# Kernel optimization log

Measured on AMD Instinct MI355X. Metric: run time of the kernel, lower is better.

## Reference

```python
import jax, jax.numpy as jnp
import numpy as np

B, T, IN, R = 256, 512, 64, 2048
SPECTRAL_RADIUS = 0.9


def setup_inputs() -> dict:
    key = jax.random.key(0)
    k1, k2 = jax.random.split(key)
    X = jax.random.normal(k1, (B, T, IN), dtype=jnp.float32)
    rng = np.random.default_rng(0)
    Win = rng.standard_normal((R, IN)).astype(np.float32)
    W = rng.standard_normal((R, R))
    eigs = np.abs(np.linalg.eigvals(W))
    W = (W / np.max(eigs) * SPECTRAL_RADIUS).astype(np.float32)
    return {"X": X, "Win": jnp.asarray(Win), "W": jnp.asarray(W)}


def reference(X, Win, W):
    def step(s, x_t):
        # s: [B, R], x_t: [B, IN]
        s_new = jnp.tanh(x_t @ Win.T + s @ W.T)
        return s_new, None

    s0 = jnp.zeros((X.shape[0], W.shape[0]), dtype=X.dtype)
    xs = jnp.swapaxes(X, 0, 1)  # [T, B, IN]
    s_final, _ = jax.lax.scan(step, s0, xs)
    return s_final  # [B, R]
```

## Files before the change

### kernel.cpp

```cpp
#include <hip/hip_runtime.h>
#include <hip/hip_fp16.h>
#include <cmath>

constexpr int kB  = 256;
constexpr int kT  = 512;
constexpr int kIN = 64;
constexpr int kR  = 2048;

constexpr int kBands  = 8;
constexpr int kNB     = 32;
constexpr int kBlocks = kBands * kNB;
constexpr int BM = 32;
constexpr int BN = 64;
constexpr int PFS = 68;

typedef _Float16 f16x8 __attribute__((ext_vector_type(8)));
typedef float    f32x4 __attribute__((ext_vector_type(4)));
typedef unsigned long long u64;

#define MFMA16(a, b, c) __builtin_amdgcn_mfma_f32_16x16x32_f16((a), (b), (c), 0, 0, 0)

__device__ __forceinline__ f16x8 cvt8(float4 a, float4 b) {
    f16x8 v;
    v[0] = (_Float16)a.x; v[1] = (_Float16)a.y; v[2] = (_Float16)a.z; v[3] = (_Float16)a.w;
    v[4] = (_Float16)b.x; v[5] = (_Float16)b.y; v[6] = (_Float16)b.z; v[7] = (_Float16)b.w;
    return v;
}

__device__ __forceinline__ unsigned get_xcc_id() {
    unsigned x;
    asm volatile("s_getreg_b32 %0, hwreg(HW_REG_XCC_ID, 0, 8)" : "=s"(x));
    return x & 0xfu;
}

__device__ __forceinline__ unsigned poll32(const unsigned* f, int lane, unsigned target) {
    unsigned v = __hip_atomic_load(f + (lane & 31), __ATOMIC_RELAXED, __HIP_MEMORY_SCOPE_AGENT);
    return (unsigned)__ballot(v >= target);
}

__global__ __launch_bounds__(512, 2) void esn_persist(
    const float* __restrict__ X,
    const float* __restrict__ Win,
    const float* __restrict__ W,
    float* __restrict__ out,
    _Float16* __restrict__ sbuf0,
    _Float16* __restrict__ sbuf1,
    unsigned* __restrict__ flags,
    unsigned* __restrict__ xcds)
{
    __shared__ __align__(16) float pf[4 * BM * PFS];
    __shared__ int fast_sh;

    const int tid  = threadIdx.x;
    const int wave = tid >> 6, lane = tid & 63;
    const int quad = lane >> 4, l16 = lane & 15;
    const int nh = wave >> 2;
    const int q  = wave & 3;
    const int mb = blockIdx.x & 7;
    const int nb = blockIdx.x >> 3;
    const int n0 = nb * BN;
    const int m0 = mb * BM;
    unsigned* bandflags = flags + mb * kNB;
    unsigned* bandxcc   = xcds  + mb * kNB;

    if (tid == 0) {
        fast_sh = 0;
        __hip_atomic_store(&bandxcc[nb], get_xcc_id() + 1u,
                           __ATOMIC_RELAXED, __HIP_MEMORY_SCOPE_AGENT);
    }

    f16x8 wfrag[2][16];
    #pragma unroll
    for (int h = 0; h < 2; ++h) {
        const float* wrow = W + (size_t)(n0 + nh * 32 + h * 16 + l16) * kR;
        #pragma unroll
        for (int j = 0; j < 16; ++j) {
            const float* p = wrow + (4 * j + q) * 32 + quad * 8;
            wfrag[h][j] = cvt8(*(const float4*)p, *(const float4*)(p + 4));
        }
    }
    f16x8 winfrag[2] = {};
    if (q < 2) {
        #pragma unroll
        for (int h = 0; h < 2; ++h) {
            const float* p = Win + (size_t)(n0 + nh * 32 + h * 16 + l16) * kIN
                           + q * 32 + quad * 8;
            winfrag[h] = cvt8(*(const float4*)p, *(const float4*)(p + 4));
        }
    }

    const size_t fbase = ((size_t)(mb * 2) * 64 + q) * 512 + quad * 128 + l16 * 8;

    const int r_   = tid >> 7;
    const int pos  = (tid & 127) * 4;
    const int mt_w = r_ >> 1, kwl = r_ & 1;
    const int l16w = (pos >> 3) & 15, qw = pos >> 7, jw = pos & 7;
    const int m_loc = mt_w * 16 + l16w;
    const int nn    = kwl * 32 + qw * 8 + jw;
    const size_t soff = ((size_t)(mb * 2 + mt_w) * 64 + (nb * 2 + kwl)) * 512 + pos;

    unsigned fastw = 0;

    #pragma unroll 1
    for (int t = 0; t < kT; ++t) {
        float4 xr[2][2];
        if (q < 2) {
            #pragma unroll
            for (int i = 0; i < 2; ++i) {
                const float* xp = X + ((size_t)(m0 + i * 16 + l16) * kT + t) * kIN
                                + q * 32 + quad * 8;
                xr[i][0] = *(const float4*)xp;
                xr[i][1] = *(const float4*)(xp + 4);
            }
        }

        f32x4 acc[2][2] = {};

        if (t > 0) {
            const _Float16* sprev = (t & 1) ? sbuf0 : sbuf1;
            const unsigned target = (unsigned)t;

            if (wave == 0) {
                unsigned fm = poll32(bandflags, lane, target);
                while (fm != 0xffffffffu) {
                    __builtin_amdgcn_s_sleep(1);
                    fm = poll32(bandflags, lane, target);
                }
                if (t == 1) {
                    const unsigned myx = get_xcc_id() + 1u;
                    unsigned px = __hip_atomic_load(bandxcc + (lane & 31),
                                                    __ATOMIC_RELAXED,
                                                    __HIP_MEMORY_SCOPE_AGENT);
                    fastw = (__ballot(px == myx) == ~0ull) ? 1u : 0u;
                    if (lane == 0) fast_sh = (int)fastw;
                }
                if (fastw && t >= 2) {
                    asm volatile("buffer_inv sc0" ::: "memory");
                } else {
                    __builtin_amdgcn_fence(__ATOMIC_ACQUIRE, "agent");
                }
            }
            __syncthreads();
            asm volatile("" ::: "memory");

            const _Float16* fp = sprev + fbase;
            f16x8 afb[2][8];

            #pragma unroll
            for (int jj = 0; jj < 4; ++jj)
                #pragma unroll
                for (int i = 0; i < 2; ++i)
                    afb[0][jj * 2 + i] = *(const f16x8*)(fp + (size_t)i * 32768
                                                         + (size_t)jj * 2048);
            #pragma unroll
            for (int g = 0; g < 4; ++g) {
                if (g + 1 < 4) {
                    #pragma unroll
                    for (int jj = 0; jj < 4; ++jj)
                        #pragma unroll
                        for (int i = 0; i < 2; ++i)
                            afb[(g + 1) & 1][jj * 2 + i] =
                                *(const f16x8*)(fp + (size_t)i * 32768
                                                + (size_t)((g + 1) * 4 + jj) * 2048);
                }
                #pragma unroll
                for (int jj = 0; jj < 4; ++jj) {
                    const int j = g * 4 + jj;
                    #pragma unroll
                    for (int i = 0; i < 2; ++i) {
                        f16x8 av = afb[g & 1][jj * 2 + i];
                        acc[i][0] = MFMA16(av, wfrag[0][j], acc[i][0]);
                        acc[i][1] = MFMA16(av, wfrag[1][j], acc[i][1]);
                    }
                }
            }
        }

        if (q < 2) {
            #pragma unroll
            for (int i = 0; i < 2; ++i) {
                f16x8 a = cvt8(xr[i][0], xr[i][1]);
                acc[i][0] = MFMA16(a, winfrag[0], acc[i][0]);
                acc[i][1] = MFMA16(a, winfrag[1], acc[i][1]);
            }
        }

        #pragma unroll
        for (int i = 0; i < 2; ++i)
            #pragma unroll
            for (int h = 0; h < 2; ++h)
                #pragma unroll
                for (int r = 0; r < 4; ++r)
                    pf[q * BM * PFS + (i * 16 + quad * 4 + r) * PFS + nh * 32 + h * 16 + l16]
                        = acc[i][h][r];
        __syncthreads();

        f32x4 v0 = *(const f32x4*)&pf[0 * BM * PFS + m_loc * PFS + nn];
        f32x4 v1 = *(const f32x4*)&pf[1 * BM * PFS + m_loc * PFS + nn];
        f32x4 v2 = *(const f32x4*)&pf[2 * BM * PFS + m_loc * PFS + nn];
        f32x4 v3 = *(const f32x4*)&pf[3 * BM * PFS + m_loc * PFS + nn];
        float o0 = tanhf(v0[0] + v1[0] + v2[0] + v3[0]);
        float o1 = tanhf(v0[1] + v1[1] + v2[1] + v3[1]);
        float o2 = tanhf(v0[2] + v1[2] + v2[2] + v3[2]);
        float o3 = tanhf(v0[3] + v1[3] + v2[3] + v3[3]);

        if (t < kT - 1) {
            _Float16* sout = (t & 1) ? sbuf1 : sbuf0;
            union { u64 u; _Float16 h[4]; } pk;
            pk.h[0] = (_Float16)o0; pk.h[1] = (_Float16)o1;
            pk.h[2] = (_Float16)o2; pk.h[3] = (_Float16)o3;
            u64* dst = (u64*)(sout + soff);
            if (fast_sh) {
                *dst = pk.u;
                asm volatile("" ::: "memory");
            } else {
                __hip_atomic_store(dst, pk.u, __ATOMIC_RELAXED,
                                   __HIP_MEMORY_SCOPE_AGENT);
            }
            __builtin_amdgcn_s_waitcnt(0);
            __syncthreads();
            if (tid == 0)
                __hip_atomic_store(&bandflags[nb], (unsigned)(t + 1),
                                   __ATOMIC_RELAXED, __HIP_MEMORY_SCOPE_AGENT);
        } else {
            float4 o; o.x = o0; o.y = o1; o.z = o2; o.w = o3;
            *(float4*)(out + (size_t)(m0 + m_loc) * kR + n0 + nn) = o;
        }
    }
}

extern "C" void kernel_launch(void* const* d_in, const int* in_sizes, int n_in,
                              void* d_out, int out_size, void* d_ws, size_t ws_size,
                              hipStream_t stream)
{
    const float* X   = (const float*)d_in[0];
    const float* Win = (const float*)d_in[1];
    const float* W   = (const float*)d_in[2];
    float* out = (float*)d_out;

    char* ws = (char*)d_ws;
    _Float16* s0 = (_Float16*)ws;
    _Float16* s1 = (_Float16*)(ws + (size_t)kB * kR * 2);
    unsigned* flags = (unsigned*)(ws + 2 * (size_t)kB * kR * 2);
    unsigned* xcds  = flags + kBands * kNB;

    hipMemsetAsync(flags, 0, 2 * kBands * kNB * sizeof(unsigned), stream);
    esn_persist<<<kBlocks, 512, 0, stream>>>(X, Win, W, out, s0, s1, flags, xcds);
}
```

Measured before the change: 2.176 ms.

## Split K across all eight waves with full-N tiles per wave

Each wave now owns a contiguous 256-wide K slice and all four 16-column N tiles, instead of two N halves crossed with a four-way K split. Every loaded state fragment feeds four MFMAs instead of two, which halves global A-fragment loads per wave. The price is a cross-wave reduction over eight partials instead of four, a doubled LDS partial buffer (about 70KB), and more accumulator registers. The larger LDS footprint may limit the two-blocks-per-CU occupancy.

```diff
diff --git a/kernel.cpp b/kernel.cpp
--- a/kernel.cpp
+++ b/kernel.cpp
@@ -48,14 +48,13 @@
     unsigned* __restrict__ flags,
     unsigned* __restrict__ xcds)
 {
-    __shared__ __align__(16) float pf[4 * BM * PFS];
+    __shared__ __align__(16) float pf[8 * BM * PFS];
     __shared__ int fast_sh;
 
     const int tid  = threadIdx.x;
     const int wave = tid >> 6, lane = tid & 63;
     const int quad = lane >> 4, l16 = lane & 15;
-    const int nh = wave >> 2;
-    const int q  = wave & 3;
+    const int q  = wave;
     const int mb = blockIdx.x & 7;
     const int nb = blockIdx.x >> 3;
     const int n0 = nb * BN;
@@ -69,27 +68,27 @@
                            __ATOMIC_RELAXED, __HIP_MEMORY_SCOPE_AGENT);
     }
 
-    f16x8 wfrag[2][16];
+    f16x8 wfrag[4][8];
     #pragma unroll
-    for (int h = 0; h < 2; ++h) {
-        const float* wrow = W + (size_t)(n0 + nh * 32 + h * 16 + l16) * kR;
-        #pragma unroll
-        for (int j = 0; j < 16; ++j) {
-            const float* p = wrow + (4 * j + q) * 32 + quad * 8;
-            wfrag[h][j] = cvt8(*(const float4*)p, *(const float4*)(p + 4));
-        }
-    }
-    f16x8 winfrag[2] = {};
+    for (int nt = 0; nt < 4; ++nt) {
+        const float* wrow = W + (size_t)(n0 + nt * 16 + l16) * kR;
+        #pragma unroll
+        for (int j = 0; j < 8; ++j) {
+            const float* p = wrow + (8 * q + j) * 32 + quad * 8;
+            wfrag[nt][j] = cvt8(*(const float4*)p, *(const float4*)(p + 4));
+        }
+    }
+    f16x8 winfrag[4] = {};
     if (q < 2) {
         #pragma unroll
-        for (int h = 0; h < 2; ++h) {
-            const float* p = Win + (size_t)(n0 + nh * 32 + h * 16 + l16) * kIN
+        for (int nt = 0; nt < 4; ++nt) {
+            const float* p = Win + (size_t)(n0 + nt * 16 + l16) * kIN
                            + q * 32 + quad * 8;
-            winfrag[h] = cvt8(*(const float4*)p, *(const float4*)(p + 4));
-        }
-    }
-
-    const size_t fbase = ((size_t)(mb * 2) * 64 + q) * 512 + quad * 128 + l16 * 8;
+            winfrag[nt] = cvt8(*(const float4*)p, *(const float4*)(p + 4));
+        }
+    }
+
+    const size_t fbase = ((size_t)(mb * 2) * 64 + 8 * q) * 512 + quad * 128 + l16 * 8;
 
     const int r_   = tid >> 7;
     const int pos  = (tid & 127) * 4;
@@ -114,7 +113,7 @@
             }
         }
 
-        f32x4 acc[2][2] = {};
+        f32x4 acc[2][4] = {};
 
         if (t > 0) {
             const _Float16* sprev = (t & 1) ? sbuf0 : sbuf1;
@@ -151,26 +150,28 @@
                 #pragma unroll
                 for (int i = 0; i < 2; ++i)
                     afb[0][jj * 2 + i] = *(const f16x8*)(fp + (size_t)i * 32768
-                                                         + (size_t)jj * 2048);
-            #pragma unroll
-            for (int g = 0; g < 4; ++g) {
-                if (g + 1 < 4) {
+                                                         + (size_t)jj * 512);
+            #pragma unroll
+            for (int g = 0; g < 2; ++g) {
+                if (g == 0) {
                     #pragma unroll
                     for (int jj = 0; jj < 4; ++jj)
                         #pragma unroll
                         for (int i = 0; i < 2; ++i)
-                            afb[(g + 1) & 1][jj * 2 + i] =
+                            afb[1][jj * 2 + i] =
                                 *(const f16x8*)(fp + (size_t)i * 32768
-                                                + (size_t)((g + 1) * 4 + jj) * 2048);
+                                                + (size_t)(4 + jj) * 512);
                 }
                 #pragma unroll
                 for (int jj = 0; jj < 4; ++jj) {
                     const int j = g * 4 + jj;
                     #pragma unroll
                     for (int i = 0; i < 2; ++i) {
-                        f16x8 av = afb[g & 1][jj * 2 + i];
+                        f16x8 av = afb[g][jj * 2 + i];
                         acc[i][0] = MFMA16(av, wfrag[0][j], acc[i][0]);
                         acc[i][1] = MFMA16(av, wfrag[1][j], acc[i][1]);
+                        acc[i][2] = MFMA16(av, wfrag[2][j], acc[i][2]);
+                        acc[i][3] = MFMA16(av, wfrag[3][j], acc[i][3]);
                     }
                 }
             }
@@ -180,29 +181,32 @@
             #pragma unroll
             for (int i = 0; i < 2; ++i) {
                 f16x8 a = cvt8(xr[i][0], xr[i][1]);
-                acc[i][0] = MFMA16(a, winfrag[0], acc[i][0]);
-                acc[i][1] = MFMA16(a, winfrag[1], acc[i][1]);
+                #pragma unroll
+                for (int nt = 0; nt < 4; ++nt)
+                    acc[i][nt] = MFMA16(a, winfrag[nt], acc[i][nt]);
             }
         }
 
         #pragma unroll
         for (int i = 0; i < 2; ++i)
             #pragma unroll
-            for (int h = 0; h < 2; ++h)
+            for (int nt = 0; nt < 4; ++nt)
                 #pragma unroll
                 for (int r = 0; r < 4; ++r)
-                    pf[q * BM * PFS + (i * 16 + quad * 4 + r) * PFS + nh * 32 + h * 16 + l16]
-                        = acc[i][h][r];
+                    pf[q * BM * PFS + (i * 16 + quad * 4 + r) * PFS + nt * 16 + l16]
+                        = acc[i][nt][r];
         __syncthreads();
 
-        f32x4 v0 = *(const f32x4*)&pf[0 * BM * PFS + m_loc * PFS + nn];
-        f32x4 v1 = *(const f32x4*)&pf[1 * BM * PFS + m_loc * PFS + nn];
-        f32x4 v2 = *(const f32x4*)&pf[2 * BM * PFS + m_loc * PFS + nn];
-        f32x4 v3 = *(const f32x4*)&pf[3 * BM * PFS + m_loc * PFS + nn];
-        float o0 = tanhf(v0[0] + v1[0] + v2[0] + v3[0]);
-        float o1 = tanhf(v0[1] + v1[1] + v2[1] + v3[1]);
-        float o2 = tanhf(v0[2] + v1[2] + v2[2] + v3[2]);
-        float o3 = tanhf(v0[3] + v1[3] + v2[3] + v3[3]);
+        f32x4 vs = {};
+        #pragma unroll
+        for (int p = 0; p < 8; ++p) {
+            f32x4 v = *(const f32x4*)&pf[p * BM * PFS + m_loc * PFS + nn];
+            vs[0] += v[0]; vs[1] += v[1]; vs[2] += v[2]; vs[3] += v[3];
+        }
+        float o0 = tanhf(vs[0]);
+        float o1 = tanhf(vs[1]);
+        float o2 = tanhf(vs[2]);
+        float o3 = tanhf(vs[3]);
 
         if (t < kT - 1) {
             _Float16* sout = (t & 1) ? sbuf1 : sbuf0;
```

Measured after the change: 1.963 ms. -9.8%, faster.
